# Optimization experiments

Measured on AMD Instinct MI355X. Metric: run time of the kernel, lower is better.

The kernel has to match this reference:

```python
import jax, jax.numpy as jnp
import numpy as np

N = 50000
E = 800000
IN_DIM = 128
HID = 128
HEADS = 8
OUT_DIM = 64
NEG_SLOPE = 0.2


def setup_inputs() -> dict:
    key = jax.random.key(0)
    ks = jax.random.split(key, 12)
    x = jax.random.normal(ks[0], (N, IN_DIM), dtype=jnp.float32)
    edge_index = jax.random.randint(ks[1], (2, E), 0, N, dtype=jnp.int64)
    C1 = HID // HEADS  # per-head out dim of layer 1
    s1 = 1.0 / np.sqrt(IN_DIM)
    s2 = 1.0 / np.sqrt(HID)
    W1 = jax.random.uniform(ks[2], (IN_DIM, HEADS * C1), jnp.float32, -s1, s1)
    a_src1 = jax.random.uniform(ks[3], (HEADS, C1), jnp.float32, -1.0, 1.0)
    a_dst1 = jax.random.uniform(ks[4], (HEADS, C1), jnp.float32, -1.0, 1.0)
    b1 = jnp.zeros((HEADS * C1,), jnp.float32)
    W2 = jax.random.uniform(ks[5], (HID, OUT_DIM), jnp.float32, -s2, s2)
    a_src2 = jax.random.uniform(ks[6], (1, OUT_DIM), jnp.float32, -1.0, 1.0)
    a_dst2 = jax.random.uniform(ks[7], (1, OUT_DIM), jnp.float32, -1.0, 1.0)
    b2 = jnp.zeros((OUT_DIM,), jnp.float32)
    return {"x": x, "edge_index": edge_index, "W1": W1, "a_src1": a_src1,
            "a_dst1": a_dst1, "b1": b1, "W2": W2, "a_src2": a_src2,
            "a_dst2": a_dst2, "b2": b2}


def gat_conv(x, src, dst, W, a_s, a_d, b, n_heads, c_head):
    # Linear projection per head: [N, H, C]
    h = (x @ W).reshape(N, n_heads, c_head)
    # Per-node attention terms: [N, H]
    alpha_s = jnp.einsum('nhc,hc->nh', h, a_s)
    alpha_d = jnp.einsum('nhc,hc->nh', h, a_d)
    # Per-edge raw scores: [Etot, H]
    score = jax.nn.leaky_relu(alpha_s[src] + alpha_d[dst], negative_slope=NEG_SLOPE)
    # Segment softmax over edges sharing the same destination
    m = jax.ops.segment_max(score, dst, num_segments=N)
    e = jnp.exp(score - m[dst])
    denom = jax.ops.segment_sum(e, dst, num_segments=N)
    alpha = e / denom[dst]  # every node has a self-loop -> denom > 0
    # Weighted aggregation: scatter-add alpha * h_src into destinations
    out = jax.ops.segment_sum(alpha[:, :, None] * h[src], dst, num_segments=N)
    return out.reshape(N, n_heads * c_head) + b


def reference(x, edge_index, W1, a_src1, a_dst1, b1, W2, a_src2, a_dst2, b2):
    # add self loops (GATConv add_self_loops=True)
    loops = jnp.arange(N, dtype=edge_index.dtype)
    src = jnp.concatenate([edge_index[0], loops])
    dst = jnp.concatenate([edge_index[1], loops])
    C1 = HID // HEADS
    h = gat_conv(x, src, dst, W1, a_src1, a_dst1, b1, HEADS, C1)
    h = jax.nn.elu(h)  # dropout = 0 (eval)
    out = gat_conv(h, src, dst, W2, a_src2, a_dst2, b2, 1, OUT_DIM)
    return jax.nn.log_softmax(out, axis=-1)
```

## Files before the change

### kernel.cpp

```cpp
#include <hip/hip_runtime.h>
#include <math.h>

typedef unsigned int  u32;
typedef unsigned short u16;
typedef unsigned char u8;
typedef short bf16x8 __attribute__((ext_vector_type(8)));
typedef float f32x4  __attribute__((ext_vector_type(4)));
typedef float f32x2  __attribute__((ext_vector_type(2)));

#define NN    50000
#define NE    800000
#define ET    (NE + NN)
#define IND   128
#define HIDD  128
#define NH    8
#define OD    64
#define SLOPE 0.2f

#define NB    196
#define EPB   4096
#define NBB   ((NE + EPB - 1) / EPB)
#define LCAP  64
#define CAPB  5120
#define CPAD  16
#define BSTRIDE 7168

#define W1EXT 144
#define W2EXT 80
#define WPB   112
#define G1B   391

__device__ __forceinline__ u32 bf16rne(float f) {
    u32 u = __float_as_uint(f);
    return (u + 0x7fffu + ((u >> 16) & 1u)) >> 16;
}

#define LR(s) fmaxf((s), SLOPE * (s))

__global__ __launch_bounds__(256) void k_prep_bin(
    const int* __restrict__ ei, int* __restrict__ cnt, u32* __restrict__ staging,
    const float* __restrict__ W1, const float* __restrict__ W2,
    const float* __restrict__ as1w, const float* __restrict__ ad1w,
    const float* __restrict__ as2w, const float* __restrict__ ad2w,
    u16* __restrict__ Wt1, u16* __restrict__ Wt2,
    u32* __restrict__ h1f8, float* __restrict__ as1, float* __restrict__ as2)
{
    __shared__ u32 lbuf[NB * LCAP];
    __shared__ int lcnt[NB];
    __shared__ int gbase[NB];
    const int t = threadIdx.x;

    if (blockIdx.x >= NBB) {
        const int i = (blockIdx.x - NBB) * 256 + t;
        if (i < 32) h1f8[(size_t)NN * 32 + i] = 0;
        if (i < 8)  as1[(size_t)NH * NN + i] = -1e30f;
        if (i == 8) as2[NN] = -1e30f;

        if (i < W1EXT * 128) {
            const int j = i >> 7, k = i & 127;
            float v;
            if (j < 128) {
                v = W1[k * 128 + j];
            } else if (j < 136) {
                const int h = j - 128;
                v = 0.f;
                for (int c = 0; c < 16; ++c)
                    v += W1[k * 128 + h * 16 + c] * as1w[h * 16 + c];
            } else {
                const int h = j - 136;
                v = 0.f;
                for (int c = 0; c < 16; ++c)
                    v += W1[k * 128 + h * 16 + c] * ad1w[h * 16 + c];
            }
            Wt1[j * 128 + k] = (u16)bf16rne(v);
        } else if (i < W1EXT * 128 + W2EXT * 128) {
            const int i2 = i - W1EXT * 128;
            const int j = i2 >> 7, k = i2 & 127;
            float v = 0.f;
            if (j < 64) {
                v = W2[k * 64 + j];
            } else if (j == 64) {
                for (int c = 0; c < 64; ++c) v += W2[k * 64 + c] * as2w[c];
            } else if (j == 65) {
                for (int c = 0; c < 64; ++c) v += W2[k * 64 + c] * ad2w[c];
            }
            Wt2[j * 128 + k] = (u16)bf16rne(v);
        }
        return;
    }

    const int e0 = blockIdx.x * EPB;
    for (int i = t; i < NB; i += 256) lcnt[i] = 0;
    __syncthreads();

    for (int i = t; i < EPB; i += 256) {
        const int e = e0 + i;
        if (e >= NE) break;
        const int src = ei[e];
        const int dst = ei[NE + e];
        const int b = dst >> 8;
        const int p = atomicAdd(&lcnt[b], 1);
        lbuf[b * LCAP + p] = ((u32)(dst & 255) << 16) | (u32)src;
    }
    __syncthreads();

    for (int i = t; i < NB; i += 256)
        gbase[i] = atomicAdd(&cnt[i * CPAD], lcnt[i]);
    __syncthreads();

    for (int b = t; b < NB; b += 256) {
        const int n = lcnt[b];
        const int gb = gbase[b];
        u32* dstp = staging + (size_t)b * CAPB + gb;
        const u32* srcp = lbuf + b * LCAP;
        for (int j = 0; j < n; ++j) dstp[j] = srcp[j];
    }
}

__global__ __launch_bounds__(512) void k_place_gemm1(
    const int* __restrict__ cnt, const u32* __restrict__ staging,
    int* __restrict__ rowptr, int* __restrict__ rowend,
    u16* __restrict__ sorted16,
    const float* __restrict__ x, const u16* __restrict__ Wt1,
    u32* __restrict__ h1f8, float* __restrict__ as1, float* __restrict__ ad1)
{
    __shared__ u32 xb[128 * 64];
    __shared__ u32 Wb[W1EXT * 64];
    const int tid = threadIdx.x;

    if (blockIdx.x < NB) {
        int* hist = (int*)xb;
        int* cur  = hist + 256;
        int* scan = cur + 256;
        const int b = blockIdx.x;
        const int tot = cnt[b * CPAD];
        const int base = b * BSTRIDE;

        if (tid < 256) hist[tid] = ((b * 256 + tid) < NN) ? 1 : 0;
        __syncthreads();

        for (int i = tid; i < tot; i += 512)
            atomicAdd(&hist[staging[(size_t)b * CAPB + i] >> 16], 1);
        __syncthreads();

        if (tid < 256) scan[tid] = (hist[tid] + 7) & ~7;
        __syncthreads();
        for (int off = 1; off < 256; off <<= 1) {
            int v = 0;
            if (tid < 256 && tid >= off) v = scan[tid - off];
            __syncthreads();
            if (tid < 256) scan[tid] += v;
            __syncthreads();
        }
        if (tid < 256) {
            const int padded = (hist[tid] + 7) & ~7;
            const int excl = (tid == 0) ? 0 : scan[tid - 1];
            const int node = b * 256 + tid;
            if (node < NN) {
                rowptr[node] = base + excl;
                rowend[node] = base + excl + padded;
                sorted16[base + excl] = (u16)node;
                for (int j = hist[tid]; j < padded; ++j)
                    sorted16[base + excl + j] = (u16)NN;
                cur[tid] = excl + 1;
            } else {
                cur[tid] = excl;
            }
        }
        __syncthreads();
        for (int i = tid; i < tot; i += 512) {
            const u32 v = staging[(size_t)b * CAPB + i];
            const int pos = atomicAdd(&cur[v >> 16], 1);
            sorted16[base + pos] = (u16)(v & 0xffffu);
        }
        return;
    }

    const int row0 = (blockIdx.x - NB) * 128;

    {
        const uint4* Wt = (const uint4*)Wt1;
        for (int p = 0; p < 5; ++p) {
            const int id = p * 512 + tid;
            if (id < W1EXT * 16) {
                const int n = id >> 4, c = id & 15;
                *(uint4*)(Wb + n * 64 + ((c ^ (n & 15)) << 2)) = Wt[n * 16 + c];
            }
        }
    }
    for (int p = 0; p < 4; ++p) {
        const int id = p * 512 + tid;
        const int m = id >> 4, c = id & 15;
        const int row = row0 + m;
        uint4 v = make_uint4(0, 0, 0, 0);
        if (row < NN) {
            const float4 f0 = *(const float4*)(x + (size_t)row * 128 + c * 8);
            const float4 f1 = *(const float4*)(x + (size_t)row * 128 + c * 8 + 4);
            v.x = bf16rne(f0.x) | (bf16rne(f0.y) << 16);
            v.y = bf16rne(f0.z) | (bf16rne(f0.w) << 16);
            v.z = bf16rne(f1.x) | (bf16rne(f1.y) << 16);
            v.w = bf16rne(f1.z) | (bf16rne(f1.w) << 16);
        }
        *(uint4*)(xb + m * 64 + ((c ^ (m & 15)) << 2)) = v;
    }
    __syncthreads();

    const int w = tid >> 6, lane = tid & 63;
    const int nl = lane & 15, quad = lane >> 4;
    f32x4 acc[9] = {};
    for (int kk = 0; kk < 4; ++kk) {
        const int cm = kk * 4 + quad;
        const bf16x8 a = *(const bf16x8*)(xb + (16 * w + nl) * 64 + ((cm ^ nl) << 2));
#pragma unroll
        for (int tn = 0; tn < 9; ++tn) {
            const bf16x8 b = *(const bf16x8*)(Wb + (16 * tn + nl) * 64 + ((cm ^ nl) << 2));
            acc[tn] = __builtin_amdgcn_mfma_f32_16x16x32_bf16(a, b, acc[tn], 0, 0, 0);
        }
    }

    __syncthreads();
    {
        u8* h1ld = (u8*)xb;
#pragma unroll
        for (int tn = 0; tn < 8; ++tn) {
#pragma unroll
            for (int r = 0; r < 4; ++r) {
                const int row = 16 * w + quad * 4 + r;
                const u32 pk = __builtin_amdgcn_cvt_pk_fp8_f32(
                    acc[tn][r], 0.f, 0u, false);
                h1ld[row * 128 + ((tn ^ ((row >> 2) & 7)) << 4) + nl] = (u8)pk;
            }
        }
    }
#pragma unroll
    for (int r = 0; r < 4; ++r) {
        const int row = row0 + 16 * w + quad * 4 + r;
        if (row < NN) {
            const float v = acc[8][r];
            if (nl < 8) as1[row * NH + nl] = v;
            else        ad1[row * NH + (nl - 8)] = v;
        }
    }
    __syncthreads();
    for (int p = 0; p < 2; ++p) {
        const int id = p * 512 + tid;
        const int row = id >> 3, c = id & 7;
        const int grow = row0 + row;
        if (grow < NN)
            ((uint4*)h1f8)[(size_t)grow * 8 + c] =
                ((const uint4*)xb)[row * 8 + (c ^ ((row >> 2) & 7))];
    }
}

__global__ __launch_bounds__(512) void k_gemm2(
    const u32* __restrict__ act2b, const u16* __restrict__ Wt2,
    u16* __restrict__ h2s, float* __restrict__ as2, float* __restrict__ ad2)
{
    __shared__ u32 xb[128 * 64];
    __shared__ u32 Wb[W2EXT * 64];
    const int tid = threadIdx.x;
    const int row0 = blockIdx.x * 128;

    {
        const uint4* Wt = (const uint4*)Wt2;
        for (int p = 0; p < 3; ++p) {
            const int id = p * 512 + tid;
            if (id < W2EXT * 16) {
                const int n = id >> 4, c = id & 15;
                *(uint4*)(Wb + n * 64 + ((c ^ (n & 15)) << 2)) = Wt[n * 16 + c];
            }
        }
    }
    for (int p = 0; p < 4; ++p) {
        const int id = p * 512 + tid;
        const int m = id >> 4, c = id & 15;
        const int row = row0 + m;
        uint4 v = make_uint4(0, 0, 0, 0);
        if (row < NN) v = ((const uint4*)act2b)[(size_t)row * 16 + c];
        *(uint4*)(xb + m * 64 + ((c ^ (m & 15)) << 2)) = v;
    }
    __syncthreads();

    const int w = tid >> 6, lane = tid & 63;
    const int nl = lane & 15, quad = lane >> 4;
    f32x4 acc[5] = {};
    for (int kk = 0; kk < 4; ++kk) {
        const int cm = kk * 4 + quad;
        const bf16x8 a = *(const bf16x8*)(xb + (16 * w + nl) * 64 + ((cm ^ nl) << 2));
#pragma unroll
        for (int tn = 0; tn < 5; ++tn) {
            const bf16x8 b = *(const bf16x8*)(Wb + (16 * tn + nl) * 64 + ((cm ^ nl) << 2));
            acc[tn] = __builtin_amdgcn_mfma_f32_16x16x32_bf16(a, b, acc[tn], 0, 0, 0);
        }
    }

    __syncthreads();
    {
        u16* h2ld = (u16*)xb;
#pragma unroll
        for (int tn = 0; tn < 4; ++tn) {
#pragma unroll
            for (int r = 0; r < 4; ++r) {
                const int row = 16 * w + quad * 4 + r;
                h2ld[row * 64 + 16 * tn + nl] = (u16)bf16rne(acc[tn][r]);
            }
        }
    }
#pragma unroll
    for (int r = 0; r < 4; ++r) {
        const int row = row0 + 16 * w + quad * 4 + r;
        if (row < NN) {
            const float v = acc[4][r];
            if (nl == 0) as2[row] = v;
            else if (nl == 1) ad2[row] = v;
        }
    }
    __syncthreads();
    for (int p = 0; p < 2; ++p) {
        const int id = p * 512 + tid;
        const int row = id >> 3, c = id & 7;
        const int grow = row0 + row;
        if (grow < NN)
            ((uint4*)h2s)[(size_t)grow * 8 + c] = ((const uint4*)xb)[row * 8 + c];
    }
}

#define PG1(KK, S, G, WJ) do {                                                \
    const uint4 p = *(const uint4*)(sorted16 + (KK));                         \
    S[0] = p.x & 0xffffu; S[1] = p.x >> 16;                                   \
    S[2] = p.y & 0xffffu; S[3] = p.y >> 16;                                   \
    S[4] = p.z & 0xffffu; S[5] = p.z >> 16;                                   \
    S[6] = p.w & 0xffffu; S[7] = p.w >> 16;                                   \
    const u32 hlf = (head & 4) ? ((head & 2) ? p.w : p.z)                     \
                               : ((head & 2) ? p.y : p.x);                    \
    const u32 sj = (head & 1) ? (hlf >> 16) : (hlf & 0xffffu);                \
    WJ = __expf(LR(as1[sj * NH + eh] + adeh));                                \
    _Pragma("unroll") for (int j = 0; j < 8; ++j)                             \
        G[j] = h1u16[S[j] * 64 + lane];                                       \
} while (0)

#define CONS1(G, WJ) do {                                                     \
    _Pragma("unroll") for (int j = 0; j < 8; ++j) {                           \
        const float wv = __uint_as_float((u32)__builtin_amdgcn_ds_bpermute(   \
            h4 + j * 32, (int)__float_as_uint(WJ)));                          \
        const f32x2 f = __builtin_amdgcn_cvt_pk_f32_fp8((u32)G[j], false);    \
        acc0 += wv * f.x;                                                     \
        acc1 += wv * f.y;                                                     \
        den  += wv; }                                                         \
} while (0)

__global__ __launch_bounds__(256) void k_agg1(
    const int* __restrict__ rowptr, const int* __restrict__ rowend,
    const u16* __restrict__ sorted16,
    const u16* __restrict__ h1u16, const float* __restrict__ as1,
    const float* __restrict__ ad1,
    u32* __restrict__ act2b)
{
    const int node = blockIdx.x * 4 + (threadIdx.x >> 6);
    const int lane = threadIdx.x & 63;
    const int head = lane >> 3;
    const int eh   = lane & 7;
    const float adeh = ad1[node * NH + eh];
    const int k0 = rowptr[node], kend = rowend[node];
    const int h4 = head << 2;
    float acc0 = 0.f, acc1 = 0.f, den = 0.f;
    u32 sA[8], sB[8];
    u16 gA[8], gB[8];
    float wA, wB;

    PG1(k0, sA, gA, wA);
    int k = k0 + 8;
    while (k + 16 <= kend) {
        PG1(k, sB, gB, wB);      CONS1(gA, wA);
        PG1(k + 8, sA, gA, wA);  CONS1(gB, wB);
        k += 16;
    }
    if (k < kend) {
        PG1(k, sB, gB, wB);  CONS1(gA, wA);  CONS1(gB, wB);
    } else {
        CONS1(gA, wA);
    }

    const float inv = 1.f / den;
    float v0 = acc0 * inv, v1 = acc1 * inv;
    v0 = v0 > 0.f ? v0 : expm1f(v0);
    v1 = v1 > 0.f ? v1 : expm1f(v1);
    act2b[node * 64 + lane] = bf16rne(v0) | (bf16rne(v1) << 16);
}

#define PG2(KK, S, G, WJ) do {                                                \
    const uint4 p = *(const uint4*)(sorted16 + (KK));                         \
    S[0] = p.x & 0xffffu; S[1] = p.x >> 16;                                   \
    S[2] = p.y & 0xffffu; S[3] = p.y >> 16;                                   \
    S[4] = p.z & 0xffffu; S[5] = p.z >> 16;                                   \
    S[6] = p.w & 0xffffu; S[7] = p.w >> 16;                                   \
    const u32 sj = (lane & 1) ? (((lane & 4) ? ((lane & 2) ? p.w : p.z)       \
                                             : ((lane & 2) ? p.y : p.x)) >> 16) \
                              : (((lane & 4) ? ((lane & 2) ? p.w : p.z)       \
                                             : ((lane & 2) ? p.y : p.x)) & 0xffffu); \
    WJ = __expf(LR(as2[sj] + adv));                                           \
    _Pragma("unroll") for (int j = 0; j < 8; ++j)                             \
        G[j] = h2s[S[j] * 64 + lane];                                         \
} while (0)

#define CONS2(G, WJ) do {                                                     \
    _Pragma("unroll") for (int j = 0; j < 8; ++j) {                           \
        const float wv = __uint_as_float((u32)__builtin_amdgcn_ds_bpermute(   \
            j << 2, (int)__float_as_uint(WJ)));                               \
        acc += wv * __uint_as_float(((u32)G[j]) << 16);                       \
        den += wv; }                                                          \
} while (0)

__global__ __launch_bounds__(256) void k_agg2(
    const int* __restrict__ rowptr, const int* __restrict__ rowend,
    const u16* __restrict__ sorted16,
    const u16* __restrict__ h2s, const float* __restrict__ as2,
    const float* __restrict__ ad2,
    float* __restrict__ out)
{
    const int node = blockIdx.x * 4 + (threadIdx.x >> 6);
    const int lane = threadIdx.x & 63;
    const float adv = ad2[node];
    const int k0 = rowptr[node], kend = rowend[node];
    float acc = 0.f, den = 0.f;
    u32 sA[8], sB[8];
    u16 gA[8], gB[8];
    float wA, wB;

    PG2(k0, sA, gA, wA);
    int k = k0 + 8;
    while (k + 16 <= kend) {
        PG2(k, sB, gB, wB);      CONS2(gA, wA);
        PG2(k + 8, sA, gA, wA);  CONS2(gB, wB);
        k += 16;
    }
    if (k < kend) {
        PG2(k, sB, gB, wB);  CONS2(gA, wA);  CONS2(gB, wB);
    } else {
        CONS2(gA, wA);
    }

    const float v = acc / den;
    float m = v;
    for (int kk = 1; kk < 64; kk <<= 1) m = fmaxf(m, __shfl_xor(m, kk));
    float se = __expf(v - m);
    for (int kk = 1; kk < 64; kk <<= 1) se += __shfl_xor(se, kk);
    out[node * 64 + lane] = v - m - logf(se);
}

extern "C" void kernel_launch(void* const* d_in, const int* in_sizes, int n_in,
                              void* d_out, int out_size, void* d_ws, size_t ws_size,
                              hipStream_t stream)
{
    (void)in_sizes; (void)n_in; (void)out_size; (void)ws_size;
    const float* x    = (const float*)d_in[0];
    const int*   ei   = (const int*)d_in[1];
    const float* W1   = (const float*)d_in[2];
    const float* as1w = (const float*)d_in[3];
    const float* ad1w = (const float*)d_in[4];
    const float* W2   = (const float*)d_in[6];
    const float* as2w = (const float*)d_in[7];
    const float* ad2w = (const float*)d_in[8];
    float* out = (float*)d_out;

    u32* ws = (u32*)d_ws;
    size_t o = 0;
    auto take = [&](size_t n) { size_t r = o; o += (n + 15) & ~(size_t)15; return r; };

    u32*   h1f8     = ws + take((size_t)32 * (NN + 1));
    float* as1      = (float*)(ws + take((size_t)NH * NN + 8));
    float* ad1      = (float*)(ws + take((size_t)NH * NN));
    u32*   act2b    = ws + take((size_t)64 * NN);
    float* as2      = (float*)(ws + take(NN + 1));
    float* ad2      = (float*)(ws + take(NN));
    int*   rowptr   = (int*)(ws + take(NN));
    int*   rowend   = (int*)(ws + take(NN));
    u16*   sorted16 = (u16*)(ws + take(((size_t)NB * BSTRIDE + 1) / 2));
    u32*   staging  = ws + take((size_t)NB * CAPB);
    int*   cnt      = (int*)(ws + take(NB * CPAD));
    u16*   Wt1      = (u16*)(ws + take((size_t)W1EXT * 128 / 2));
    u16*   Wt2      = (u16*)(ws + take((size_t)W2EXT * 128 / 2));
    u16*   h1u16    = (u16*)h1f8;
    u16*   h2s      = (u16*)h1f8;

    hipMemsetAsync(cnt, 0, NB * CPAD * sizeof(int), stream);

    k_prep_bin<<<NBB + WPB, 256, 0, stream>>>(
        ei, cnt, staging, W1, W2, as1w, ad1w, as2w, ad2w,
        Wt1, Wt2, h1f8, as1, as2);

    k_place_gemm1<<<NB + G1B, 512, 0, stream>>>(
        cnt, staging, rowptr, rowend, sorted16, x, Wt1, h1f8, as1, ad1);

    k_agg1<<<NN / 4, 256, 0, stream>>>(rowptr, rowend, sorted16, h1u16, as1, ad1, act2b);
    k_gemm2<<<G1B, 512, 0, stream>>>(act2b, Wt2, h2s, as2, ad2);
    k_agg2<<<NN / 4, 256, 0, stream>>>(rowptr, rowend, sorted16, h2s, as2, ad2, out);
}
```

Measured before the change: 179.1 us.

## Split layer-1 features into two head slices for cache-friendlier aggregation

Stores the fp8 layer-1 features and the per-head attention terms as two separate slices of four heads each. The first aggregation kernel now runs two blocks per node group, one per slice, and each wavefront splits its 8 edges into two halves that are combined with a cross-half shuffle. The aim is to halve the gathered working set per pass so the random source-row gathers fit better in cache. The cost is twice the blocks, a reduction shuffle, and half the lanes idle at the final store.

```diff
diff --git a/kernel.cpp b/kernel.cpp
--- a/kernel.cpp
+++ b/kernel.cpp
@@ -30,12 +30,20 @@
 #define WPB   112
 #define G1B   391
 
+#define SSTR ((size_t)(NN + 1) * 16)
+#define ASTR ((size_t)(NN + 1) * 4)
+
 __device__ __forceinline__ u32 bf16rne(float f) {
     u32 u = __float_as_uint(f);
     return (u + 0x7fffu + ((u >> 16) & 1u)) >> 16;
 }
 
 #define LR(s) fmaxf((s), SLOPE * (s))
+
+__device__ __forceinline__ u32 sel8(uint4 p, int e) {
+    const u32 c = (e & 4) ? ((e & 2) ? p.w : p.z) : ((e & 2) ? p.y : p.x);
+    return (e & 1) ? (c >> 16) : (c & 0xffffu);
+}
 
 __global__ __launch_bounds__(256) void k_prep_bin(
     const int* __restrict__ ei, int* __restrict__ cnt, u32* __restrict__ staging,
@@ -43,7 +51,7 @@
     const float* __restrict__ as1w, const float* __restrict__ ad1w,
     const float* __restrict__ as2w, const float* __restrict__ ad2w,
     u16* __restrict__ Wt1, u16* __restrict__ Wt2,
-    u32* __restrict__ h1f8, float* __restrict__ as1, float* __restrict__ as2)
+    u32* __restrict__ h1s8, float* __restrict__ as1s, float* __restrict__ as2)
 {
     __shared__ u32 lbuf[NB * LCAP];
     __shared__ int lcnt[NB];
@@ -52,8 +60,10 @@
 
     if (blockIdx.x >= NBB) {
         const int i = (blockIdx.x - NBB) * 256 + t;
-        if (i < 32) h1f8[(size_t)NN * 32 + i] = 0;
-        if (i < 8)  as1[(size_t)NH * NN + i] = -1e30f;
+        if (i < 32)
+            h1s8[(size_t)(i >> 4) * SSTR + (size_t)NN * 16 + (i & 15)] = 0;
+        if (i < 8)
+            as1s[(size_t)(i >> 2) * ASTR + (size_t)NN * 4 + (i & 3)] = -1e30f;
         if (i == 8) as2[NN] = -1e30f;
 
         if (i < W1EXT * 128) {
@@ -122,7 +132,7 @@
     int* __restrict__ rowptr, int* __restrict__ rowend,
     u16* __restrict__ sorted16,
     const float* __restrict__ x, const u16* __restrict__ Wt1,
-    u32* __restrict__ h1f8, float* __restrict__ as1, float* __restrict__ ad1)
+    u32* __restrict__ h1s8, float* __restrict__ as1s, float* __restrict__ ad1s)
 {
     __shared__ u32 xb[128 * 64];
     __shared__ u32 Wb[W1EXT * 64];
@@ -237,8 +247,12 @@
         const int row = row0 + 16 * w + quad * 4 + r;
         if (row < NN) {
             const float v = acc[8][r];
-            if (nl < 8) as1[row * NH + nl] = v;
-            else        ad1[row * NH + (nl - 8)] = v;
+            if (nl < 8)
+                as1s[(size_t)(nl >> 2) * ASTR + (size_t)row * 4 + (nl & 3)] = v;
+            else {
+                const int h = nl - 8;
+                ad1s[(size_t)(h >> 2) * ASTR + (size_t)row * 4 + (h & 3)] = v;
+            }
         }
     }
     __syncthreads();
@@ -247,8 +261,9 @@
         const int row = id >> 3, c = id & 7;
         const int grow = row0 + row;
         if (grow < NN)
-            ((uint4*)h1f8)[(size_t)grow * 8 + c] =
-                ((const uint4*)xb)[row * 8 + (c ^ ((row >> 2) & 7))];
+            ((uint4*)h1s8)[(size_t)(c >> 2) * ((size_t)(NN + 1) * 4) +
+                           (size_t)grow * 4 + (c & 3)]
+                = ((const uint4*)xb)[row * 8 + (c ^ ((row >> 2) & 7))];
     }
 }
 
@@ -325,67 +340,72 @@
     }
 }
 
-#define PG1(KK, S, G, WJ) do {                                                \
+#define PG1(KK, G, WJ) do {                                                   \
     const uint4 p = *(const uint4*)(sorted16 + (KK));                         \
-    S[0] = p.x & 0xffffu; S[1] = p.x >> 16;                                   \
-    S[2] = p.y & 0xffffu; S[3] = p.y >> 16;                                   \
-    S[4] = p.z & 0xffffu; S[5] = p.z >> 16;                                   \
-    S[6] = p.w & 0xffffu; S[7] = p.w >> 16;                                   \
-    const u32 hlf = (head & 4) ? ((head & 2) ? p.w : p.z)                     \
-                               : ((head & 2) ? p.y : p.x);                    \
-    const u32 sj = (head & 1) ? (hlf >> 16) : (hlf & 0xffffu);                \
-    WJ = __expf(LR(as1[sj * NH + eh] + adeh));                                \
-    _Pragma("unroll") for (int j = 0; j < 8; ++j)                             \
-        G[j] = h1u16[S[j] * 64 + lane];                                       \
+    const u32 se = sel8(p, eidx);                                             \
+    WJ = __expf(LR(asl[(size_t)se * 4 + ehead] + adeh));                      \
+    _Pragma("unroll") for (int i = 0; i < 4; ++i) {                           \
+        const u32 si = sel8(p, 2 * i + half);                                 \
+        G[i] = h1u[(size_t)si * 32 + chp]; }                                  \
 } while (0)
 
 #define CONS1(G, WJ) do {                                                     \
-    _Pragma("unroll") for (int j = 0; j < 8; ++j) {                           \
+    _Pragma("unroll") for (int i = 0; i < 4; ++i) {                           \
         const float wv = __uint_as_float((u32)__builtin_amdgcn_ds_bpermute(   \
-            h4 + j * 32, (int)__float_as_uint(WJ)));                          \
-        const f32x2 f = __builtin_amdgcn_cvt_pk_f32_fp8((u32)G[j], false);    \
-        acc0 += wv * f.x;                                                     \
-        acc1 += wv * f.y;                                                     \
-        den  += wv; }                                                         \
+            bpb + 32 * i, (int)__float_as_uint(WJ)));                         \
+        const f32x2 f = __builtin_amdgcn_cvt_pk_f32_fp8((u32)G[i], false);    \
+        acc0 += wv * f.x; acc1 += wv * f.y; den += wv; }                      \
 } while (0)
 
 __global__ __launch_bounds__(256) void k_agg1(
     const int* __restrict__ rowptr, const int* __restrict__ rowend,
     const u16* __restrict__ sorted16,
-    const u16* __restrict__ h1u16, const float* __restrict__ as1,
-    const float* __restrict__ ad1,
+    const u16* __restrict__ h1u16, const float* __restrict__ as1s,
+    const float* __restrict__ ad1s,
     u32* __restrict__ act2b)
 {
-    const int node = blockIdx.x * 4 + (threadIdx.x >> 6);
+    const int b = blockIdx.x;
+    const int slice = b & 1;
+    const int node = (b >> 1) * 4 + (threadIdx.x >> 6);
     const int lane = threadIdx.x & 63;
-    const int head = lane >> 3;
-    const int eh   = lane & 7;
-    const float adeh = ad1[node * NH + eh];
+    const int half = lane >> 5;
+    const int chp  = lane & 31;
+    const int myhead = chp >> 3;
+    const int ehead = lane & 3;
+    const int eidx  = (lane >> 2) & 7;
+    const int bpb   = ((half << 2) | myhead) << 2;
+    const float* asl = as1s + (size_t)slice * ASTR;
+    const float adeh = ad1s[(size_t)slice * ASTR + (size_t)node * 4 + ehead];
+    const u16* h1u = h1u16 + (size_t)slice * (size_t)(NN + 1) * 32;
     const int k0 = rowptr[node], kend = rowend[node];
-    const int h4 = head << 2;
     float acc0 = 0.f, acc1 = 0.f, den = 0.f;
-    u32 sA[8], sB[8];
-    u16 gA[8], gB[8];
+    u16 gA[4], gB[4];
     float wA, wB;
 
-    PG1(k0, sA, gA, wA);
+    PG1(k0, gA, wA);
     int k = k0 + 8;
     while (k + 16 <= kend) {
-        PG1(k, sB, gB, wB);      CONS1(gA, wA);
-        PG1(k + 8, sA, gA, wA);  CONS1(gB, wB);
+        PG1(k, gB, wB);      CONS1(gA, wA);
+        PG1(k + 8, gA, wA);  CONS1(gB, wB);
         k += 16;
     }
     if (k < kend) {
-        PG1(k, sB, gB, wB);  CONS1(gA, wA);  CONS1(gB, wB);
+        PG1(k, gB, wB);  CONS1(gA, wA);  CONS1(gB, wB);
     } else {
         CONS1(gA, wA);
     }
+
+    acc0 += __shfl_xor(acc0, 32);
+    acc1 += __shfl_xor(acc1, 32);
+    den  += __shfl_xor(den, 32);
 
     const float inv = 1.f / den;
     float v0 = acc0 * inv, v1 = acc1 * inv;
     v0 = v0 > 0.f ? v0 : expm1f(v0);
     v1 = v1 > 0.f ? v1 : expm1f(v1);
-    act2b[node * 64 + lane] = bf16rne(v0) | (bf16rne(v1) << 16);
+    if (lane < 32)
+        act2b[(size_t)node * 64 + slice * 32 + chp] =
+            bf16rne(v0) | (bf16rne(v1) << 16);
 }
 
 #define PG2(KK, S, G, WJ) do {                                                \
@@ -394,10 +414,7 @@
     S[2] = p.y & 0xffffu; S[3] = p.y >> 16;                                   \
     S[4] = p.z & 0xffffu; S[5] = p.z >> 16;                                   \
     S[6] = p.w & 0xffffu; S[7] = p.w >> 16;                                   \
-    const u32 sj = (lane & 1) ? (((lane & 4) ? ((lane & 2) ? p.w : p.z)       \
-                                             : ((lane & 2) ? p.y : p.x)) >> 16) \
-                              : (((lane & 4) ? ((lane & 2) ? p.w : p.z)       \
-                                             : ((lane & 2) ? p.y : p.x)) & 0xffffu); \
+    const u32 sj = sel8(p, lane & 7);                                         \
     WJ = __expf(LR(as2[sj] + adv));                                           \
     _Pragma("unroll") for (int j = 0; j < 8; ++j)                             \
         G[j] = h2s[S[j] * 64 + lane];                                         \
@@ -467,9 +484,9 @@
     size_t o = 0;
     auto take = [&](size_t n) { size_t r = o; o += (n + 15) & ~(size_t)15; return r; };
 
-    u32*   h1f8     = ws + take((size_t)32 * (NN + 1));
-    float* as1      = (float*)(ws + take((size_t)NH * NN + 8));
-    float* ad1      = (float*)(ws + take((size_t)NH * NN));
+    u32*   h1s8     = ws + take(2 * SSTR);
+    float* as1s     = (float*)(ws + take(2 * ASTR));
+    float* ad1s     = (float*)(ws + take(2 * ASTR));
     u32*   act2b    = ws + take((size_t)64 * NN);
     float* as2      = (float*)(ws + take(NN + 1));
     float* ad2      = (float*)(ws + take(NN));
@@ -480,19 +497,19 @@
     int*   cnt      = (int*)(ws + take(NB * CPAD));
     u16*   Wt1      = (u16*)(ws + take((size_t)W1EXT * 128 / 2));
     u16*   Wt2      = (u16*)(ws + take((size_t)W2EXT * 128 / 2));
-    u16*   h1u16    = (u16*)h1f8;
-    u16*   h2s      = (u16*)h1f8;
+    u16*   h1u16    = (u16*)h1s8;
+    u16*   h2s      = (u16*)h1s8;
 
     hipMemsetAsync(cnt, 0, NB * CPAD * sizeof(int), stream);
 
     k_prep_bin<<<NBB + WPB, 256, 0, stream>>>(
         ei, cnt, staging, W1, W2, as1w, ad1w, as2w, ad2w,
-        Wt1, Wt2, h1f8, as1, as2);
+        Wt1, Wt2, h1s8, as1s, as2);
 
     k_place_gemm1<<<NB + G1B, 512, 0, stream>>>(
-        cnt, staging, rowptr, rowend, sorted16, x, Wt1, h1f8, as1, ad1);
-
-    k_agg1<<<NN / 4, 256, 0, stream>>>(rowptr, rowend, sorted16, h1u16, as1, ad1, act2b);
+        cnt, staging, rowptr, rowend, sorted16, x, Wt1, h1s8, as1s, ad1s);
+
+    k_agg1<<<NN / 2, 256, 0, stream>>>(rowptr, rowend, sorted16, h1u16, as1s, ad1s, act2b);
     k_gemm2<<<G1B, 512, 0, stream>>>(act2b, Wt2, h2s, as2, ad2);
     k_agg2<<<NN / 4, 256, 0, stream>>>(rowptr, rowend, sorted16, h2s, as2, ad2, out);
 }
```

Result: slower. 194.0 us (+8.3%).
